# Kernel optimization log

Measured on AMD Instinct MI355X. Metric: run time of the kernel, lower is better.

## Reference

```python
import math
import jax, jax.numpy as jnp
import numpy as np

HIDDEN = 1024
NUM_HEADS = 16
NUM_QUERIES = 2
NUM_Q_HEADS = NUM_HEADS * NUM_QUERIES  # 32
HEAD_DIM = 64
Q_DIM = NUM_Q_HEADS * HEAD_DIM   # 2048
KV_DIM = NUM_HEADS * HEAD_DIM    # 1024
BATCH, SEQ = 4, 1024


def _alibi_slopes(num_heads: int) -> np.ndarray:
    # num_heads is a power of two here, so only the main branch applies
    closest_pow2 = 2 ** int(math.floor(math.log2(num_heads)))
    base = 2.0 ** (-(2.0 ** (-(math.log2(closest_pow2) - 3))))
    powers = np.arange(1, closest_pow2 + 1, dtype=np.float32)
    slopes = base ** powers
    if closest_pow2 != num_heads:
        extra_base = 2.0 ** (-(2.0 ** (-(math.log2(2 * closest_pow2) - 3))))
        extra_powers = np.arange(1, 2 * (num_heads - closest_pow2) + 1, 2, dtype=np.float32)
        slopes = np.concatenate([slopes, extra_base ** extra_powers])
    return slopes[:num_heads].astype(np.float32)

ALIBI_SLOPES = jnp.asarray(_alibi_slopes(NUM_Q_HEADS))  # (32,)


def setup_inputs() -> dict:
    key = jax.random.key(0)
    k1, k2, k3 = jax.random.split(key, 3)
    inputs = jax.random.normal(k1, (BATCH, SEQ, HIDDEN), dtype=jnp.float32)
    # match nn.Linear default init scale roughly
    W_qkv = jax.random.normal(k2, (HIDDEN, Q_DIM + 2 * KV_DIM), dtype=jnp.float32) * (1.0 / math.sqrt(HIDDEN))
    W_out = jax.random.normal(k3, (Q_DIM, HIDDEN), dtype=jnp.float32) * (1.0 / math.sqrt(Q_DIM))
    return {"inputs": inputs, "W_qkv": W_qkv, "W_out": W_out}


def reference(inputs, W_qkv, W_out):
    B, S, _ = inputs.shape
    qkv = inputs @ W_qkv                                   # [B,S,4096]
    q = qkv[..., :Q_DIM].reshape(B, S, NUM_Q_HEADS, HEAD_DIM).transpose(0, 2, 1, 3)   # [B,32,S,64]
    k = qkv[..., Q_DIM:Q_DIM + KV_DIM].reshape(B, S, NUM_HEADS, HEAD_DIM).transpose(0, 2, 1, 3)
    v = qkv[..., Q_DIM + KV_DIM:].reshape(B, S, NUM_HEADS, HEAD_DIM).transpose(0, 2, 1, 3)
    # GQA: repeat_interleave along head dim
    k = jnp.repeat(k, NUM_QUERIES, axis=1)                 # [B,32,S,64]
    v = jnp.repeat(v, NUM_QUERIES, axis=1)
    # ALiBi bias: slope_h * (kv_pos - q_pos)
    pos = jnp.arange(S)
    rel = (pos[None, :] - pos[:, None]).astype(jnp.float32)           # [S,S]
    bias = ALIBI_SLOPES[:, None, None] * rel[None, :, :]              # [32,S,S]
    scores = jnp.einsum('bhqd,bhkd->bhqk', q, k) / math.sqrt(HEAD_DIM)
    scores = scores + bias[None]
    causal = pos[:, None] >= pos[None, :]                             # [S,S]
    scores = jnp.where(causal[None, None], scores, -jnp.inf)
    attn = jax.nn.softmax(scores, axis=-1)
    out = jnp.einsum('bhqk,bhkd->bhqd', attn, v)                      # [B,32,S,64]
    out = out.transpose(0, 2, 1, 3).reshape(B, S, Q_DIM)
    return out @ W_out                                                # [B,S,HIDDEN]
```

## Files before the change

### kernel.cpp

```cpp
#include <hip/hip_runtime.h>

typedef unsigned short u16;
typedef float f32x4 __attribute__((ext_vector_type(4)));
typedef __bf16 bf16x8 __attribute__((ext_vector_type(8)));
typedef short short8 __attribute__((ext_vector_type(8)));
typedef u16 u16x4 __attribute__((ext_vector_type(4)));
typedef float f32x4v __attribute__((ext_vector_type(4)));

#define DEV __device__ __forceinline__

DEV u16 f2bf(float f) {
    union { float f; unsigned u; } v; v.f = f;
    unsigned r = v.u + 0x7FFFu + ((v.u >> 16) & 1u);
    return (u16)(r >> 16);
}

DEV void gload_lds16(const u16* g, u16* l) {
    __builtin_amdgcn_global_load_lds(
        (const __attribute__((address_space(1))) void*)g,
        (__attribute__((address_space(3))) void*)l, 16, 0, 0);
}

__global__ __launch_bounds__(256) void k_cvt(const float* __restrict__ in,
                                             u16* __restrict__ out, int n4) {
    int i = blockIdx.x * 256 + threadIdx.x;
    if (i >= n4) return;
    f32x4v v = reinterpret_cast<const f32x4v*>(in)[i];
    u16x4 o;
    o.x = f2bf(v.x); o.y = f2bf(v.y); o.z = f2bf(v.z); o.w = f2bf(v.w);
    reinterpret_cast<u16x4*>(out)[i] = o;
}

__global__ __launch_bounds__(256) void k_transpose_cvt(const float* __restrict__ in,
                                                       u16* __restrict__ out,
                                                       int R, int C) {
    __shared__ float tile[32][33];
    const int c0 = blockIdx.x * 32, r0 = blockIdx.y * 32;
    const int tx = threadIdx.x & 31, ty = threadIdx.x >> 5;
#pragma unroll
    for (int i = 0; i < 32; i += 8)
        tile[ty + i][tx] = in[(size_t)(r0 + ty + i) * C + c0 + tx];
    __syncthreads();
#pragma unroll
    for (int i = 0; i < 32; i += 8)
        out[(size_t)(c0 + ty + i) * R + r0 + tx] = f2bf(tile[tx][ty + i]);
}

template <int OUTF>
__global__ __launch_bounds__(256) void k_gemm_nt(const u16* __restrict__ A,
                                                 const u16* __restrict__ Bt,
                                                 void* __restrict__ Cv,
                                                 int M, int N, int K) {
    __shared__ u16 lA[2][4096];
    __shared__ u16 lB[2][4096];
    const int t = threadIdx.x, l = t & 63, w = t >> 6;
    const int bm = blockIdx.y * 128, bn = blockIdx.x * 128;
    const int wr = w >> 1, wc = w & 1;
    const int lm = l & 15, lg = l >> 4;

    f32x4 acc[4][4] = {};

    const int nk = K >> 5;
    auto stage = [&](int buf, int kt) {
        const int k0 = kt << 5;
        const int kc = (l & 3) * 8;
        const int rsub = w * 16 + (l >> 2);
#pragma unroll
        for (int p = 0; p < 2; ++p) {
            const int row = p * 64 + rsub;
            gload_lds16(A + (size_t)(bm + row) * K + k0 + kc, &lA[buf][p * 2048 + w * 512]);
            gload_lds16(Bt + (size_t)(bn + row) * K + k0 + kc, &lB[buf][p * 2048 + w * 512]);
        }
    };

    stage(0, 0);
    __syncthreads();
    for (int kt = 0; kt < nk; ++kt) {
        const int buf = kt & 1;
        if (kt + 1 < nk) stage(buf ^ 1, kt + 1);
        bf16x8 af[4], bfr[4];
#pragma unroll
        for (int i = 0; i < 4; ++i) {
            af[i]  = *reinterpret_cast<const bf16x8*>(&lA[buf][(wr * 64 + i * 16 + lm) * 32 + lg * 8]);
            bfr[i] = *reinterpret_cast<const bf16x8*>(&lB[buf][(wc * 64 + i * 16 + lm) * 32 + lg * 8]);
        }
        __builtin_amdgcn_s_setprio(1);
#pragma unroll
        for (int mi = 0; mi < 4; ++mi)
#pragma unroll
            for (int ni = 0; ni < 4; ++ni)
                acc[mi][ni] = __builtin_amdgcn_mfma_f32_16x16x32_bf16(af[mi], bfr[ni], acc[mi][ni], 0, 0, 0);
        __builtin_amdgcn_s_setprio(0);
        __syncthreads();
    }

#pragma unroll
    for (int mi = 0; mi < 4; ++mi)
#pragma unroll
        for (int ni = 0; ni < 4; ++ni)
#pragma unroll
            for (int r = 0; r < 4; ++r) {
                const int row = bm + wr * 64 + mi * 16 + lg * 4 + r;
                const int col = bn + wc * 64 + ni * 16 + lm;
                if (OUTF)
                    reinterpret_cast<float*>(Cv)[(size_t)row * N + col] = acc[mi][ni][r];
                else
                    reinterpret_cast<u16*>(Cv)[(size_t)row * N + col] = f2bf(acc[mi][ni][r]);
            }
}

__global__ __launch_bounds__(256) void k_attn(const u16* __restrict__ qkv,
                                              u16* __restrict__ AO) {
    __shared__ u16 lK[4096];
    __shared__ u16 lVT[4096];
    __shared__ u16 lP[4][2048];

    const int t = threadIdx.x, l = t & 63, w = t >> 6;
    const int lm = l & 15, lg = l >> 4;
    const int qb = blockIdx.x;
    const int hq = blockIdx.y;
    const int b  = blockIdx.z;
    const int hkv = hq >> 1;
    const float slope = exp2f(-0.25f * (float)(hq + 1));

    const size_t RS = 4096;
    const u16* Qg = qkv + (size_t)(b * 1024 + qb * 128) * RS + hq * 64;
    const u16* Kg = qkv + (size_t)(b * 1024) * RS + 2048 + hkv * 64;
    const u16* Vg = qkv + (size_t)(b * 1024) * RS + 3072 + hkv * 64;

    bf16x8 aq[2][2];
#pragma unroll
    for (int qf = 0; qf < 2; ++qf)
#pragma unroll
        for (int ks = 0; ks < 2; ++ks)
            aq[qf][ks] = *reinterpret_cast<const bf16x8*>(
                Qg + (size_t)(w * 32 + qf * 16 + lm) * RS + ks * 32 + lg * 8);

    float m_s[2][4], l_s[2][4];
    f32x4 acc_o[2][4] = {};
#pragma unroll
    for (int qf = 0; qf < 2; ++qf)
#pragma unroll
        for (int r = 0; r < 4; ++r) { m_s[qf][r] = -1e30f; l_s[qf][r] = 0.f; }

    const int kbmax = qb * 2 + 1;
    const int qmax = qb * 128 + w * 32 + 31;

    for (int kb = 0; kb <= kbmax; ++kb) {
        {
            const int rr = w * 8 + (l >> 3);
            const int ch = l & 7;
#pragma unroll
            for (int p = 0; p < 2; ++p) {
                const int row = p * 32 + rr;
                const int sc_ = ch ^ (row & 7);
                gload_lds16(Kg + (size_t)(kb * 64 + row) * RS + sc_ * 8,
                            &lK[p * 2048 + w * 512]);
            }
        }
        {
#pragma unroll
            for (int p = 0; p < 2; ++p) {
                const int kv = p * 32 + (t >> 3);
                const int d0 = (t & 7) * 8;
                short8 v = *reinterpret_cast<const short8*>(Vg + (size_t)(kb * 64 + kv) * RS + d0);
#pragma unroll
                for (int j = 0; j < 8; ++j) {
                    const int d = d0 + j;
                    const int key = (d ^ (d >> 3)) & 7;
                    lVT[d * 64 + (((kv >> 3) ^ key) & 7) * 8 + (kv & 7)] = (u16)v[j];
                }
            }
        }
        __syncthreads();

        if (kb * 64 <= qmax) {
            f32x4 sc[2][4] = {};
#pragma unroll
            for (int ks = 0; ks < 2; ++ks) {
                bf16x8 bk[4];
#pragma unroll
                for (int kf = 0; kf < 4; ++kf) {
                    const int row = kf * 16 + lm;
                    bk[kf] = *reinterpret_cast<const bf16x8*>(
                        &lK[row * 64 + (((ks * 4 + lg) ^ (row & 7)) & 7) * 8]);
                }
                __builtin_amdgcn_s_setprio(1);
#pragma unroll
                for (int qf = 0; qf < 2; ++qf)
#pragma unroll
                    for (int kf = 0; kf < 4; ++kf)
                        sc[qf][kf] = __builtin_amdgcn_mfma_f32_16x16x32_bf16(aq[qf][ks], bk[kf], sc[qf][kf], 0, 0, 0);
                __builtin_amdgcn_s_setprio(0);
            }
#pragma unroll
            for (int qf = 0; qf < 2; ++qf) {
#pragma unroll
                for (int r = 0; r < 4; ++r) {
                    const int q = qb * 128 + w * 32 + qf * 16 + lg * 4 + r;
                    float vals[4];
                    float mx = -1e30f;
#pragma unroll
                    for (int kf = 0; kf < 4; ++kf) {
                        const int kv = kb * 64 + kf * 16 + lm;
                        float v = sc[qf][kf][r] * 0.125f + slope * (float)(kv - q);
                        if (kv > q) v = -1e30f;
                        vals[kf] = v;
                        mx = fmaxf(mx, v);
                    }
                    mx = fmaxf(mx, __shfl_xor(mx, 1));
                    mx = fmaxf(mx, __shfl_xor(mx, 2));
                    mx = fmaxf(mx, __shfl_xor(mx, 4));
                    mx = fmaxf(mx, __shfl_xor(mx, 8));
                    const float mold = m_s[qf][r];
                    const float mnew = fmaxf(mold, mx);
                    const float scl = __expf(mold - mnew);
                    m_s[qf][r] = mnew;
                    float ps = 0.f;
                    const int qloc = qf * 16 + lg * 4 + r;
                    const int key = qloc & 7;
#pragma unroll
                    for (int kf = 0; kf < 4; ++kf) {
                        float p = __expf(vals[kf] - mnew);
                        ps += p;
                        lP[w][qloc * 64 + (((kf * 2 + (lm >> 3)) ^ key) & 7) * 8 + (lm & 7)] = f2bf(p);
                    }
                    ps += __shfl_xor(ps, 1);
                    ps += __shfl_xor(ps, 2);
                    ps += __shfl_xor(ps, 4);
                    ps += __shfl_xor(ps, 8);
                    l_s[qf][r] = l_s[qf][r] * scl + ps;
#pragma unroll
                    for (int df = 0; df < 4; ++df)
                        acc_o[qf][df][r] *= scl;
                }
            }
            asm volatile("s_waitcnt lgkmcnt(0)" ::: "memory");
#pragma unroll
            for (int ks = 0; ks < 2; ++ks) {
                bf16x8 ap[2], bv[4];
#pragma unroll
                for (int qf = 0; qf < 2; ++qf) {
                    const int row = qf * 16 + lm;
                    ap[qf] = *reinterpret_cast<const bf16x8*>(
                        &lP[w][row * 64 + (((ks * 4 + lg) ^ (row & 7)) & 7) * 8]);
                }
#pragma unroll
                for (int df = 0; df < 4; ++df) {
                    const int d = df * 16 + lm;
                    const int key = (d ^ (d >> 3)) & 7;
                    bv[df] = *reinterpret_cast<const bf16x8*>(
                        &lVT[d * 64 + (((ks * 4 + lg) ^ key) & 7) * 8]);
                }
                __builtin_amdgcn_s_setprio(1);
#pragma unroll
                for (int qf = 0; qf < 2; ++qf)
#pragma unroll
                    for (int df = 0; df < 4; ++df)
                        acc_o[qf][df] = __builtin_amdgcn_mfma_f32_16x16x32_bf16(ap[qf], bv[df], acc_o[qf][df], 0, 0, 0);
                __builtin_amdgcn_s_setprio(0);
            }
        }
        __syncthreads();
    }

#pragma unroll
    for (int qf = 0; qf < 2; ++qf)
#pragma unroll
        for (int r = 0; r < 4; ++r) {
            const float invl = 1.f / l_s[qf][r];
            const int q = qb * 128 + w * 32 + qf * 16 + lg * 4 + r;
#pragma unroll
            for (int df = 0; df < 4; ++df)
                AO[(size_t)(b * 1024 + q) * 2048 + hq * 64 + df * 16 + lm] = f2bf(acc_o[qf][df][r] * invl);
        }
}

extern "C" void kernel_launch(void* const* d_in, const int* in_sizes, int n_in,
                              void* d_out, int out_size, void* d_ws, size_t ws_size,
                              hipStream_t stream) {
    const float* X    = (const float*)d_in[0];
    const float* Wqkv = (const float*)d_in[1];
    const float* Wout = (const float*)d_in[2];
    float* out = (float*)d_out;

    char* ws = (char*)d_ws;
    u16* Xb    = (u16*)(ws);
    u16* WqkvT = (u16*)(ws + (size_t)(8  << 20));
    u16* WoutT = (u16*)(ws + (size_t)(16 << 20));
    u16* QKV   = (u16*)(ws + (size_t)(20 << 20));
    u16* AO    = (u16*)(ws + (size_t)(52 << 20));

    k_cvt<<<4096, 256, 0, stream>>>(X, Xb, (4096 * 1024) / 4);
    k_transpose_cvt<<<dim3(128, 32), 256, 0, stream>>>(Wqkv, WqkvT, 1024, 4096);
    k_transpose_cvt<<<dim3(32, 64), 256, 0, stream>>>(Wout, WoutT, 2048, 1024);

    k_gemm_nt<0><<<dim3(32, 32), 256, 0, stream>>>(Xb, WqkvT, QKV, 4096, 4096, 1024);

    k_attn<<<dim3(8, 32, 4), 256, 0, stream>>>(QKV, AO);

    k_gemm_nt<1><<<dim3(8, 32), 256, 0, stream>>>(AO, WoutT, out, 4096, 1024, 2048);
}
```

Measured before the change: 299.1 us.

## Rewrite attention with 32x32 MFMA, S-transposed register-resident P, 512-thread blocks

The attention kernel now uses 32x32x16 bf16 MFMAs that compute S transposed (K as the A operand, Q as B). Each lane then holds a full query column, so the row max and sum need only one cross-lane shuffle. P is converted in registers with v_cvt_pk_bf16_f32 and fed straight into the PV MFMA, with V rows permuted to match, instead of going through LDS. Softmax moves to the exp2 domain with folded scale and slope constants. Blocks grow to 512 threads covering 256 queries, which halves the block count and increases K/V reuse, at the cost of more register pressure and coarser causal load balance.

```diff
diff --git a/kernel.cpp b/kernel.cpp
--- a/kernel.cpp
+++ b/kernel.cpp
@@ -1,7 +1,9 @@
 #include <hip/hip_runtime.h>
 
 typedef unsigned short u16;
+typedef unsigned int u32;
 typedef float f32x4 __attribute__((ext_vector_type(4)));
+typedef float f32x16 __attribute__((ext_vector_type(16)));
 typedef __bf16 bf16x8 __attribute__((ext_vector_type(8)));
 typedef short short8 __attribute__((ext_vector_type(8)));
 typedef u16 u16x4 __attribute__((ext_vector_type(4)));
@@ -109,171 +111,171 @@
             }
 }
 
-__global__ __launch_bounds__(256) void k_attn(const u16* __restrict__ qkv,
-                                              u16* __restrict__ AO) {
+__global__ __launch_bounds__(512, 4) void k_attn(const u16* __restrict__ qkv,
+                                                 u16* __restrict__ AO) {
     __shared__ u16 lK[4096];
     __shared__ u16 lVT[4096];
-    __shared__ u16 lP[4][2048];
+    __shared__ float lSc[8][32];
 
     const int t = threadIdx.x, l = t & 63, w = t >> 6;
-    const int lm = l & 15, lg = l >> 4;
+    const int lo5 = l & 31, hi = l >> 5;
     const int qb = blockIdx.x;
     const int hq = blockIdx.y;
     const int b  = blockIdx.z;
     const int hkv = hq >> 1;
-    const float slope = exp2f(-0.25f * (float)(hq + 1));
-
+    const float L2E = 1.44269504088896f;
+    const float slope2 = exp2f(-0.25f * (float)(hq + 1)) * L2E;
+    const float scale2 = 0.125f * L2E;
     const size_t RS = 4096;
-    const u16* Qg = qkv + (size_t)(b * 1024 + qb * 128) * RS + hq * 64;
+    const u16* Qg = qkv + (size_t)(b * 1024 + qb * 256) * RS + hq * 64;
     const u16* Kg = qkv + (size_t)(b * 1024) * RS + 2048 + hkv * 64;
     const u16* Vg = qkv + (size_t)(b * 1024) * RS + 3072 + hkv * 64;
 
-    bf16x8 aq[2][2];
-#pragma unroll
-    for (int qf = 0; qf < 2; ++qf)
-#pragma unroll
-        for (int ks = 0; ks < 2; ++ks)
-            aq[qf][ks] = *reinterpret_cast<const bf16x8*>(
-                Qg + (size_t)(w * 32 + qf * 16 + lm) * RS + ks * 32 + lg * 8);
-
-    float m_s[2][4], l_s[2][4];
-    f32x4 acc_o[2][4] = {};
-#pragma unroll
-    for (int qf = 0; qf < 2; ++qf)
-#pragma unroll
-        for (int r = 0; r < 4; ++r) { m_s[qf][r] = -1e30f; l_s[qf][r] = 0.f; }
-
-    const int kbmax = qb * 2 + 1;
-    const int qmax = qb * 128 + w * 32 + 31;
-
-    for (int kb = 0; kb <= kbmax; ++kb) {
+    const int q = qb * 256 + w * 32 + lo5;
+
+    bf16x8 qfr[4];
+#pragma unroll
+    for (int ks = 0; ks < 4; ++ks)
+        qfr[ks] = *reinterpret_cast<const bf16x8*>(
+            Qg + (size_t)(w * 32 + lo5) * RS + ks * 16 + hi * 8);
+
+    f32x16 acc0 = {}, acc1 = {};
+    float m_ = -3.0e38f, l_ = 0.f;
+
+    const int nt = (qb + 1) * 4;
+    const int kbd = (qb * 256 + w * 32 + 31) >> 6;
+
+    for (int kb = 0; kb < nt; ++kb) {
         {
-            const int rr = w * 8 + (l >> 3);
-            const int ch = l & 7;
-#pragma unroll
-            for (int p = 0; p < 2; ++p) {
-                const int row = p * 32 + rr;
-                const int sc_ = ch ^ (row & 7);
-                gload_lds16(Kg + (size_t)(kb * 64 + row) * RS + sc_ * 8,
-                            &lK[p * 2048 + w * 512]);
-            }
+            const int row = t >> 3;
+            const int ch = (t & 7) ^ (row & 7);
+            gload_lds16(Kg + (size_t)(kb * 64 + row) * RS + ch * 8, &lK[w * 512]);
         }
         {
-#pragma unroll
-            for (int p = 0; p < 2; ++p) {
-                const int kv = p * 32 + (t >> 3);
-                const int d0 = (t & 7) * 8;
-                short8 v = *reinterpret_cast<const short8*>(Vg + (size_t)(kb * 64 + kv) * RS + d0);
-#pragma unroll
-                for (int j = 0; j < 8; ++j) {
-                    const int d = d0 + j;
-                    const int key = (d ^ (d >> 3)) & 7;
-                    lVT[d * 64 + (((kv >> 3) ^ key) & 7) * 8 + (kv & 7)] = (u16)v[j];
+            const int kv = t >> 3, d0 = (t & 7) * 8;
+            short8 v = *reinterpret_cast<const short8*>(Vg + (size_t)(kb * 64 + kv) * RS + d0);
+            const int kvs = (kv & ~12) | ((kv & 4) << 1) | ((kv & 8) >> 1);
+#pragma unroll
+            for (int j = 0; j < 8; ++j) {
+                const int d = d0 + j;
+                const int key = (d ^ (d >> 3)) & 7;
+                lVT[d * 64 + (((kvs >> 3) ^ key) & 7) * 8 + (kvs & 7)] = (u16)v[j];
+            }
+        }
+        __syncthreads();
+
+        if (kb <= kbd) {
+            f32x16 sc0 = {}, sc1 = {};
+#pragma unroll
+            for (int ks = 0; ks < 4; ++ks) {
+                const int csw = ((ks * 2 + hi) ^ (lo5 & 7)) * 8;
+                bf16x8 ka0 = *reinterpret_cast<const bf16x8*>(&lK[lo5 * 64 + csw]);
+                bf16x8 ka1 = *reinterpret_cast<const bf16x8*>(&lK[(32 + lo5) * 64 + csw]);
+                __builtin_amdgcn_s_setprio(1);
+                sc0 = __builtin_amdgcn_mfma_f32_32x32x16_bf16(ka0, qfr[ks], sc0, 0, 0, 0);
+                sc1 = __builtin_amdgcn_mfma_f32_32x32x16_bf16(ka1, qfr[ks], sc1, 0, 0, 0);
+                __builtin_amdgcn_s_setprio(0);
+            }
+            float s[32];
+            const float b0 = slope2 * (float)(kb * 64 + 4 * hi - q);
+            const float b1 = slope2 * (float)(kb * 64 + 32 + 4 * hi - q);
+#pragma unroll
+            for (int r = 0; r < 16; ++r) {
+                const int Cr = (r & 3) + 8 * (r >> 2);
+                s[r]      = fmaf(sc0[r], scale2, fmaf(slope2, (float)Cr, b0));
+                s[16 + r] = fmaf(sc1[r], scale2, fmaf(slope2, (float)Cr, b1));
+            }
+            if (kb == kbd) {
+                const int qr0 = q - kb * 64 - 4 * hi;
+#pragma unroll
+                for (int r = 0; r < 16; ++r) {
+                    const int Cr = (r & 3) + 8 * (r >> 2);
+                    if (Cr > qr0)      s[r]      = -3.0e38f;
+                    if (Cr + 32 > qr0) s[16 + r] = -3.0e38f;
                 }
             }
-        }
-        __syncthreads();
-
-        if (kb * 64 <= qmax) {
-            f32x4 sc[2][4] = {};
-#pragma unroll
-            for (int ks = 0; ks < 2; ++ks) {
-                bf16x8 bk[4];
-#pragma unroll
-                for (int kf = 0; kf < 4; ++kf) {
-                    const int row = kf * 16 + lm;
-                    bk[kf] = *reinterpret_cast<const bf16x8*>(
-                        &lK[row * 64 + (((ks * 4 + lg) ^ (row & 7)) & 7) * 8]);
+            float tm[16];
+#pragma unroll
+            for (int i = 0; i < 16; ++i) tm[i] = fmaxf(s[i], s[16 + i]);
+#pragma unroll
+            for (int i = 0; i < 8; ++i) tm[i] = fmaxf(tm[i], tm[8 + i]);
+#pragma unroll
+            for (int i = 0; i < 4; ++i) tm[i] = fmaxf(tm[i], tm[4 + i]);
+            float mx = fmaxf(fmaxf(tm[0], tm[1]), fmaxf(tm[2], tm[3]));
+            mx = fmaxf(mx, __shfl_xor(mx, 32));
+            const float mnew = fmaxf(m_, mx);
+            const float sclf = exp2f(m_ - mnew);
+            m_ = mnew;
+#pragma unroll
+            for (int i = 0; i < 32; ++i) s[i] = exp2f(s[i] - mnew);
+            float ts[16];
+#pragma unroll
+            for (int i = 0; i < 16; ++i) ts[i] = s[i] + s[16 + i];
+#pragma unroll
+            for (int i = 0; i < 8; ++i) ts[i] += ts[8 + i];
+#pragma unroll
+            for (int i = 0; i < 4; ++i) ts[i] += ts[4 + i];
+            float sum = (ts[0] + ts[1]) + (ts[2] + ts[3]);
+            sum += __shfl_xor(sum, 32);
+            l_ = l_ * sclf + sum;
+            lSc[w][lo5] = sclf;
+            asm volatile("s_waitcnt lgkmcnt(0)" ::: "memory");
+            float rs_[16];
+#pragma unroll
+            for (int r = 0; r < 16; ++r) {
+                const int Cr = (r & 3) + 8 * (r >> 2);
+                rs_[r] = lSc[w][Cr + 4 * hi];
+            }
+#pragma unroll
+            for (int r = 0; r < 16; ++r) { acc0[r] *= rs_[r]; acc1[r] *= rs_[r]; }
+            u32 pw[16];
+#pragma unroll
+            for (int s4 = 0; s4 < 4; ++s4) {
+                const int off = (s4 >> 1) * 16 + (s4 & 1) * 8;
+#pragma unroll
+                for (int j = 0; j < 4; ++j) {
+                    u32 o;
+                    asm("v_cvt_pk_bf16_f32 %0, %1, %2"
+                        : "=v"(o) : "v"(s[off + 2 * j]), "v"(s[off + 2 * j + 1]));
+                    pw[s4 * 4 + j] = o;
                 }
+            }
+            const int key0 = (lo5 ^ (lo5 >> 3)) & 7;
+            const int key1 = ((32 + lo5) ^ ((32 + lo5) >> 3)) & 7;
+#pragma unroll
+            for (int s4 = 0; s4 < 4; ++s4) {
+                bf16x8 pa;
+                u32* paw = reinterpret_cast<u32*>(&pa);
+                paw[0] = pw[s4 * 4 + 0]; paw[1] = pw[s4 * 4 + 1];
+                paw[2] = pw[s4 * 4 + 2]; paw[3] = pw[s4 * 4 + 3];
+                const int cl = s4 * 2 + hi;
+                bf16x8 va0 = *reinterpret_cast<const bf16x8*>(&lVT[lo5 * 64 + ((cl ^ key0) & 7) * 8]);
+                bf16x8 va1 = *reinterpret_cast<const bf16x8*>(&lVT[(32 + lo5) * 64 + ((cl ^ key1) & 7) * 8]);
                 __builtin_amdgcn_s_setprio(1);
-#pragma unroll
-                for (int qf = 0; qf < 2; ++qf)
-#pragma unroll
-                    for (int kf = 0; kf < 4; ++kf)
-                        sc[qf][kf] = __builtin_amdgcn_mfma_f32_16x16x32_bf16(aq[qf][ks], bk[kf], sc[qf][kf], 0, 0, 0);
-                __builtin_amdgcn_s_setprio(0);
-            }
-#pragma unroll
-            for (int qf = 0; qf < 2; ++qf) {
-#pragma unroll
-                for (int r = 0; r < 4; ++r) {
-                    const int q = qb * 128 + w * 32 + qf * 16 + lg * 4 + r;
-                    float vals[4];
-                    float mx = -1e30f;
-#pragma unroll
-                    for (int kf = 0; kf < 4; ++kf) {
-                        const int kv = kb * 64 + kf * 16 + lm;
-                        float v = sc[qf][kf][r] * 0.125f + slope * (float)(kv - q);
-                        if (kv > q) v = -1e30f;
-                        vals[kf] = v;
-                        mx = fmaxf(mx, v);
-                    }
-                    mx = fmaxf(mx, __shfl_xor(mx, 1));
-                    mx = fmaxf(mx, __shfl_xor(mx, 2));
-                    mx = fmaxf(mx, __shfl_xor(mx, 4));
-                    mx = fmaxf(mx, __shfl_xor(mx, 8));
-                    const float mold = m_s[qf][r];
-                    const float mnew = fmaxf(mold, mx);
-                    const float scl = __expf(mold - mnew);
-                    m_s[qf][r] = mnew;
-                    float ps = 0.f;
-                    const int qloc = qf * 16 + lg * 4 + r;
-                    const int key = qloc & 7;
-#pragma unroll
-                    for (int kf = 0; kf < 4; ++kf) {
-                        float p = __expf(vals[kf] - mnew);
-                        ps += p;
-                        lP[w][qloc * 64 + (((kf * 2 + (lm >> 3)) ^ key) & 7) * 8 + (lm & 7)] = f2bf(p);
-                    }
-                    ps += __shfl_xor(ps, 1);
-                    ps += __shfl_xor(ps, 2);
-                    ps += __shfl_xor(ps, 4);
-                    ps += __shfl_xor(ps, 8);
-                    l_s[qf][r] = l_s[qf][r] * scl + ps;
-#pragma unroll
-                    for (int df = 0; df < 4; ++df)
-                        acc_o[qf][df][r] *= scl;
-                }
-            }
-            asm volatile("s_waitcnt lgkmcnt(0)" ::: "memory");
-#pragma unroll
-            for (int ks = 0; ks < 2; ++ks) {
-                bf16x8 ap[2], bv[4];
-#pragma unroll
-                for (int qf = 0; qf < 2; ++qf) {
-                    const int row = qf * 16 + lm;
-                    ap[qf] = *reinterpret_cast<const bf16x8*>(
-                        &lP[w][row * 64 + (((ks * 4 + lg) ^ (row & 7)) & 7) * 8]);
-                }
-#pragma unroll
-                for (int df = 0; df < 4; ++df) {
-                    const int d = df * 16 + lm;
-                    const int key = (d ^ (d >> 3)) & 7;
-                    bv[df] = *reinterpret_cast<const bf16x8*>(
-                        &lVT[d * 64 + (((ks * 4 + lg) ^ key) & 7) * 8]);
-                }
-                __builtin_amdgcn_s_setprio(1);
-#pragma unroll
-                for (int qf = 0; qf < 2; ++qf)
-#pragma unroll
-                    for (int df = 0; df < 4; ++df)
-                        acc_o[qf][df] = __builtin_amdgcn_mfma_f32_16x16x32_bf16(ap[qf], bv[df], acc_o[qf][df], 0, 0, 0);
+                acc0 = __builtin_amdgcn_mfma_f32_32x32x16_bf16(pa, va0, acc0, 0, 0, 0);
+                acc1 = __builtin_amdgcn_mfma_f32_32x32x16_bf16(pa, va1, acc1, 0, 0, 0);
                 __builtin_amdgcn_s_setprio(0);
             }
         }
         __syncthreads();
     }
 
-#pragma unroll
-    for (int qf = 0; qf < 2; ++qf)
-#pragma unroll
-        for (int r = 0; r < 4; ++r) {
-            const float invl = 1.f / l_s[qf][r];
-            const int q = qb * 128 + w * 32 + qf * 16 + lg * 4 + r;
-#pragma unroll
-            for (int df = 0; df < 4; ++df)
-                AO[(size_t)(b * 1024 + q) * 2048 + hq * 64 + df * 16 + lm] = f2bf(acc_o[qf][df][r] * invl);
-        }
+    lSc[w][lo5] = 1.0f / l_;
+    asm volatile("s_waitcnt lgkmcnt(0)" ::: "memory");
+    float rl[16];
+#pragma unroll
+    for (int r = 0; r < 16; ++r) {
+        const int Cr = (r & 3) + 8 * (r >> 2);
+        rl[r] = lSc[w][Cr + 4 * hi];
+    }
+    u16* AOp = AO + (size_t)(b * 1024 + qb * 256 + w * 32) * 2048 + hq * 64;
+#pragma unroll
+    for (int r = 0; r < 16; ++r) {
+        const int Cr = (r & 3) + 8 * (r >> 2);
+        const size_t rowoff = (size_t)(Cr + 4 * hi) * 2048;
+        AOp[rowoff + lo5]      = f2bf(acc0[r] * rl[r]);
+        AOp[rowoff + 32 + lo5] = f2bf(acc1[r] * rl[r]);
+    }
 }
 
 extern "C" void kernel_launch(void* const* d_in, const int* in_sizes, int n_in,
@@ -297,7 +299,7 @@
 
     k_gemm_nt<0><<<dim3(32, 32), 256, 0, stream>>>(Xb, WqkvT, QKV, 4096, 4096, 1024);
 
-    k_attn<<<dim3(8, 32, 4), 256, 0, stream>>>(QKV, AO);
+    k_attn<<<dim3(4, 32, 4), 512, 0, stream>>>(QKV, AO);
 
     k_gemm_nt<1><<<dim3(8, 32), 256, 0, stream>>>(AO, WoutT, out, 4096, 1024, 2048);
 }
```

Result: faster. 284.6 us (-4.9%).
